# Performance work log

Hardware: AMD Instinct MI355X
Metric: run time of the kernel (lower is better)

## Reference

```python
import jax, jax.numpy as jnp
import numpy as np


def setup_inputs() -> dict:
    key = jax.random.key(0)
    k1, k2 = jax.random.split(key)
    b, feat = 8192, 256
    x = jax.random.normal(k1, (b, feat), dtype=jnp.float32)
    y = jax.random.randint(k2, (b,), 0, 100, dtype=jnp.int64)
    T = jnp.zeros((1,), dtype=jnp.float32)
    return {"x": x, "y": y, "T": T}


def reference(x, y, T):
    # SNNLoss.forward with inv=False, d=None, and no -1 labels in y
    b = x.shape[0]
    x = x / jnp.std(x, ddof=1)  # torch .std() is unbiased (ddof=1)

    # Pairwise Euclidean distance via Gram matrix (avoids [b,b,feat] blowup)
    sq = jnp.sum(x * x, axis=1)  # [b]
    d2 = jnp.maximum(sq[:, None] + sq[None, :] - 2.0 * (x @ x.T), 0.0)  # [b,b]
    eye = jnp.eye(b, dtype=bool)
    # diagonal is exactly 0 and masked out later; keep sqrt grad-safe there
    dist = jnp.where(eye, 0.0, jnp.sqrt(jnp.where(eye, 1.0, d2)))

    e_dist = -dist * jnp.power(jnp.float32(10.0), T[0])  # [b,b]
    neg_inf = jnp.float32(-jnp.inf)

    # denominator: all pairs except self
    den_dist = jnp.where(eye, neg_inf, e_dist)
    den = jax.scipy.special.logsumexp(den_dist, axis=1)  # [b]

    # numerator: same-label pairs except self
    m_num = (y[:, None] == y[None, :]) & ~eye  # [b,b]
    has = jnp.any(m_num, axis=1)  # rows with at least one positive
    num_dist = jnp.where(m_num, e_dist, neg_inf)
    # rows with no positives would give logsumexp = -inf; torch code zeroes
    # both num and den there. Substitute finite values, then zero the term.
    num = jax.scipy.special.logsumexp(jnp.where(has[:, None], num_dist, 0.0), axis=1)
    terms = jnp.where(has, num - den, 0.0)
    return -jnp.mean(terms)
```

## Files before the change

### kernel.cpp

```cpp
#include <hip/hip_runtime.h>

#define B_ROWS 8192
#define FEAT   256
#define NBLK   512
#define NJTILE 128

typedef float f32x4 __attribute__((ext_vector_type(4)));
typedef _Float16 f16x8 __attribute__((ext_vector_type(8)));

typedef const __attribute__((address_space(1))) unsigned int* gas_ptr;
typedef __attribute__((address_space(3))) unsigned int* las_ptr;

__device__ __forceinline__ void gload_lds16(const void* g, void* l) {
  __builtin_amdgcn_global_load_lds((gas_ptr)g, (las_ptr)l, 16, 0, 0);
}

__device__ __forceinline__ int Rc(int it) { return it * (129 - it); }

__global__ __launch_bounds__(256) void prep_kernel(
    const float* __restrict__ x, unsigned short* __restrict__ xh,
    float* __restrict__ sq, float* __restrict__ part_s,
    float* __restrict__ part_q, float* __restrict__ col_den,
    float* __restrict__ col_num, float* __restrict__ row_den,
    float* __restrict__ row_num)
{
  int tid = threadIdx.x;
  int l = tid & 63, wid = tid >> 6;
  int row = blockIdx.x * 4 + wid;
  const float4* xv = (const float4*)(x + (size_t)row * FEAT);
  float4 v = xv[l];
  ushort4 u;
  u.x = __builtin_bit_cast(unsigned short, (_Float16)v.x);
  u.y = __builtin_bit_cast(unsigned short, (_Float16)v.y);
  u.z = __builtin_bit_cast(unsigned short, (_Float16)v.z);
  u.w = __builtin_bit_cast(unsigned short, (_Float16)v.w);
  size_t off = ((size_t)(row >> 4) * 8 + (l >> 3)) * 1024
             + ((l >> 1) & 3) * 256 + (row & 15) * 16 + (l & 1) * 8;
  *(ushort4*)((char*)xh + off) = u;
  if (tid < 4) {
    int r4 = blockIdx.x * 4 + tid;
    col_den[r4] = 0.f; col_num[r4] = 0.f;
    row_den[r4] = 0.f; row_num[r4] = 0.f;
  }
  float ssq  = v.x*v.x + v.y*v.y + v.z*v.z + v.w*v.w;
  float ssum = v.x + v.y + v.z + v.w;
  #pragma unroll
  for (int m = 32; m; m >>= 1) {
    ssq  += __shfl_xor(ssq, m);
    ssum += __shfl_xor(ssum, m);
  }
  if (l == 0) sq[row] = ssq;
  __shared__ float red[8];
  if (l == 0) { red[wid*2] = ssum; red[wid*2+1] = ssq; }
  __syncthreads();
  if (tid == 0) {
    part_s[blockIdx.x] = red[0]+red[2]+red[4]+red[6];
    part_q[blockIdx.x] = red[1]+red[3]+red[5]+red[7];
  }
}

template<bool DIAG>
__device__ __forceinline__ void epilogue(
    const f32x4 (&acc)[2][4], const float* __restrict__ sq,
    const int* __restrict__ y, int j0, int l15, int l,
    int rbase, const float (&sqi)[8], const int (&yiv)[8],
    float (&sden)[8], float (&snum)[8], float nscale2,
    float* __restrict__ col_den, float* __restrict__ col_num)
{
  int jb = j0 + l15;
  float sqj[4]; int yj[4];
  #pragma unroll
  for (int cb = 0; cb < 4; ++cb) {
    int j = jb + cb*16;
    sqj[cb] = sq[j];
    yj[cb]  = y[j];
  }
  float cd[4], cn[4];
  if (!DIAG) {
    #pragma unroll
    for (int cb = 0; cb < 4; ++cb) { cd[cb] = 0.f; cn[cb] = 0.f; }
  }
  #pragma unroll
  for (int rb = 0; rb < 2; ++rb) {
    #pragma unroll
    for (int r = 0; r < 4; ++r) {
      float si = sqi[rb*4+r];
      int   ig = rbase + rb*16 + r;
      int   yi = yiv[rb*4+r];
      float dacc = 0.f, nacc = 0.f;
      #pragma unroll
      for (int cb = 0; cb < 4; ++cb) {
        float S  = acc[rb][cb][r];
        float d2 = fmaf(S, -2.0f, si + sqj[cb]);
        d2 = fmaxf(d2, 0.0f);
        float e  = __builtin_amdgcn_exp2f(__builtin_amdgcn_sqrtf(d2) * nscale2);
        bool same = (yi == yj[cb]);
        bool offd = !DIAG || (ig != jb + cb*16);
        dacc += offd ? e : 0.0f;
        nacc += (same && offd) ? e : 0.0f;
        if (!DIAG) {
          cd[cb] += e;
          cn[cb] += same ? e : 0.0f;
        }
      }
      sden[rb*4+r] += dacc;
      snum[rb*4+r] += nacc;
    }
  }
  if (!DIAG) {
    #pragma unroll
    for (int cb = 0; cb < 4; ++cb) {
      cd[cb] += __shfl_xor(cd[cb], 16);
      cd[cb] += __shfl_xor(cd[cb], 32);
      cn[cb] += __shfl_xor(cn[cb], 16);
      cn[cb] += __shfl_xor(cn[cb], 32);
    }
    if (l < 16) {
      #pragma unroll
      for (int cb = 0; cb < 4; ++cb) {
        atomicAdd(&col_den[j0 + cb*16 + l], cd[cb]);
        atomicAdd(&col_num[j0 + cb*16 + l], cn[cb]);
      }
    }
  }
}

__device__ __forceinline__ void process_run(
    int it, int jt0, int nt, const char* __restrict__ xb,
    const float* __restrict__ sq, const int* __restrict__ y,
    float nscale2, int l, int wid, int quad, int l15,
    float* __restrict__ row_den, float* __restrict__ row_num,
    float* __restrict__ col_den, float* __restrict__ col_num,
    char* lB)
{
  f16x8 areg[2][8];
  #pragma unroll
  for (int rb = 0; rb < 2; ++rb)
    #pragma unroll
    for (int kk = 0; kk < 8; ++kk)
      areg[rb][kk] = *(const f16x8*)(xb +
          ((size_t)(it*8 + wid*2 + rb) * 8 + kk) * 1024 + l*16);

  float sqi[8]; int yiv[8];
  int rbase = it*128 + wid*32 + quad*4;
  #pragma unroll
  for (int rb = 0; rb < 2; ++rb)
    #pragma unroll
    for (int r = 0; r < 4; ++r) {
      int idx = rbase + rb*16 + r;
      sqi[rb*4+r] = sq[idx];
      yiv[rb*4+r] = y[idx];
    }

  float sden[8], snum[8];
  #pragma unroll
  for (int v = 0; v < 8; ++v) { sden[v] = 0.f; snum[v] = 0.f; }
  f32x4 acc[2][4];
  const f32x4 zero4 = {0.f, 0.f, 0.f, 0.f};

  for (int n = 0; n < nt; ++n) {
    int jt = jt0 + n;

    __syncthreads();
    {
      const char* gB = xb + (size_t)jt * 32768;
      #pragma unroll
      for (int s = 0; s < 8; ++s) {
        int cc = wid*8 + s;
        gload_lds16(gB + cc*1024 + l*16, lB + cc*1024);
      }
    }

    if (n > 0) {
      int pjt = jt - 1;
      if ((pjt >> 1) == it)
        epilogue<true >(acc, sq, y, pjt*64, l15, l, rbase, sqi, yiv,
                        sden, snum, nscale2, col_den, col_num);
      else
        epilogue<false>(acc, sq, y, pjt*64, l15, l, rbase, sqi, yiv,
                        sden, snum, nscale2, col_den, col_num);
    }
    #pragma unroll
    for (int rb = 0; rb < 2; ++rb)
      #pragma unroll
      for (int cb = 0; cb < 4; ++cb)
        acc[rb][cb] = zero4;

    __syncthreads();

    #pragma unroll
    for (int kk = 0; kk < 8; ++kk) {
      f16x8 bv[4];
      #pragma unroll
      for (int cb = 0; cb < 4; ++cb)
        bv[cb] = *(const f16x8*)(lB + (cb*8 + kk)*1024 + l*16);
      #pragma unroll
      for (int rb = 0; rb < 2; ++rb)
        #pragma unroll
        for (int cb = 0; cb < 4; ++cb)
          acc[rb][cb] = __builtin_amdgcn_mfma_f32_16x16x32_f16(areg[rb][kk], bv[cb], acc[rb][cb], 0, 0, 0);
    }
  }
  {
    int pjt = jt0 + nt - 1;
    if ((pjt >> 1) == it)
      epilogue<true >(acc, sq, y, pjt*64, l15, l, rbase, sqi, yiv,
                      sden, snum, nscale2, col_den, col_num);
    else
      epilogue<false>(acc, sq, y, pjt*64, l15, l, rbase, sqi, yiv,
                      sden, snum, nscale2, col_den, col_num);
  }

  #pragma unroll
  for (int v = 0; v < 8; ++v) {
    #pragma unroll
    for (int m = 1; m <= 8; m <<= 1) {
      sden[v] += __shfl_xor(sden[v], m);
      snum[v] += __shfl_xor(snum[v], m);
    }
  }
  if (l15 == 0) {
    #pragma unroll
    for (int rb = 0; rb < 2; ++rb)
      #pragma unroll
      for (int r = 0; r < 4; ++r) {
        int ig = rbase + rb*16 + r;
        atomicAdd(&row_den[ig], sden[rb*4+r]);
        atomicAdd(&row_num[ig], snum[rb*4+r]);
      }
  }
}

__global__ __launch_bounds__(256, 2) void snn_main(
    const unsigned short* __restrict__ xh, const float* __restrict__ sq,
    const int* __restrict__ y, const float* __restrict__ T,
    const float* __restrict__ part_s, const float* __restrict__ part_q,
    float* __restrict__ row_den, float* __restrict__ row_num,
    float* __restrict__ col_den, float* __restrict__ col_num)
{
  __shared__ __align__(16) char lB[32768];
  int tid = threadIdx.x;
  int l = tid & 63, wid = tid >> 6;
  int quad = l >> 4, l15 = l & 15;
  int b = blockIdx.x;
  const char* xb = (const char*)xh;

  float s_acc = 0.f, q_acc = 0.f;
  #pragma unroll
  for (int t = 0; t < 32; ++t) {
    s_acc += part_s[l + 64*t];
    q_acc += part_q[l + 64*t];
  }
  #pragma unroll
  for (int m = 1; m <= 32; m <<= 1) {
    s_acc += __shfl_xor(s_acc, m);
    q_acc += __shfl_xor(q_acc, m);
  }
  const double n = (double)B_ROWS * FEAT;
  double var = ((double)q_acc - (double)s_acc*(double)s_acc/n) / (n - 1.0);
  float stdv = (float)sqrt(var);
  float p10  = __builtin_amdgcn_exp2f(T[0] * 3.3219280948873623f);
  float nscale2 = -(p10 * 1.4426950408889634f / stdv);

  int k    = (b * 65) >> 3;
  int kend = ((b + 1) * 65) >> 3;
  int it = (int)((129.0f - __builtin_amdgcn_sqrtf(16641.0f - 4.0f*(float)k)) * 0.5f);
  if (it < 0) it = 0;
  if (it > 63) it = 63;
  while (it < 63 && Rc(it + 1) <= k) ++it;
  while (it > 0 && Rc(it) > k) --it;

  while (k < kend) {
    int jt0  = 2*it + (k - Rc(it));
    int rowe = Rc(it + 1);
    int stop = (kend < rowe) ? kend : rowe;
    int nt   = stop - k;
    process_run(it, jt0, nt, xb, sq, y, nscale2, l, wid, quad, l15,
                row_den, row_num, col_den, col_num, lB);
    k = stop;
    ++it;
  }
}

__global__ __launch_bounds__(1024) void final_kernel(
    const float* __restrict__ row_den, const float* __restrict__ row_num,
    const float* __restrict__ col_den, const float* __restrict__ col_num,
    float* __restrict__ out)
{
  int tid = threadIdx.x;
  float tot = 0.f;
  #pragma unroll
  for (int rr = 0; rr < 8; ++rr) {
    int row = tid + 1024*rr;
    float den = row_den[row] + col_den[row];
    float num = row_num[row] + col_num[row];
    if (num > 0.f)
      tot += 0.6931471805599453f *
             (__builtin_amdgcn_logf(num) - __builtin_amdgcn_logf(den));
  }
  #pragma unroll
  for (int m = 32; m; m >>= 1) tot += __shfl_xor(tot, m);
  __shared__ float red[16];
  if ((tid & 63) == 0) red[tid >> 6] = tot;
  __syncthreads();
  if (tid == 0) {
    float s = 0.f;
    #pragma unroll
    for (int w = 0; w < 16; ++w) s += red[w];
    out[0] = -s / 8192.0f;
  }
}

extern "C" void kernel_launch(void* const* d_in, const int* in_sizes, int n_in,
                              void* d_out, int out_size, void* d_ws, size_t ws_size,
                              hipStream_t stream)
{
  (void)in_sizes; (void)n_in; (void)out_size; (void)ws_size;
  const float* x  = (const float*)d_in[0];
  const int* y    = (const int*)d_in[1];
  const float* T  = (const float*)d_in[2];
  char* ws = (char*)d_ws;
  float* part_s = (float*)(ws + 1024);
  float* part_q = (float*)(ws + 1024 + 8192);
  float* sq     = (float*)(ws + 32768);
  unsigned short* xh = (unsigned short*)(ws + 65536);
  float* col_den = (float*)(ws + 65536 + 4194304);
  float* col_num = col_den + B_ROWS;
  float* row_den = col_num + B_ROWS;
  float* row_num = row_den + B_ROWS;

  hipLaunchKernelGGL(prep_kernel, dim3(B_ROWS/4), dim3(256), 0, stream,
                     x, xh, sq, part_s, part_q, col_den, col_num,
                     row_den, row_num);
  hipLaunchKernelGGL(snn_main, dim3(NBLK), dim3(256), 0, stream,
                     xh, sq, y, T, part_s, part_q, row_den, row_num,
                     col_den, col_num);
  hipLaunchKernelGGL(final_kernel, dim3(1), dim3(1024), 0, stream,
                     row_den, row_num, col_den, col_num, (float*)d_out);
}
```

Before: 106.3 us.

## Fuse prep, main and final kernels into one persistent kernel with grid barriers

```diff
diff --git a/kernel.cpp b/kernel.cpp
--- a/kernel.cpp
+++ b/kernel.cpp
@@ -16,48 +16,6 @@
 }
 
 __device__ __forceinline__ int Rc(int it) { return it * (129 - it); }
-
-__global__ __launch_bounds__(256) void prep_kernel(
-    const float* __restrict__ x, unsigned short* __restrict__ xh,
-    float* __restrict__ sq, float* __restrict__ part_s,
-    float* __restrict__ part_q, float* __restrict__ col_den,
-    float* __restrict__ col_num, float* __restrict__ row_den,
-    float* __restrict__ row_num)
-{
-  int tid = threadIdx.x;
-  int l = tid & 63, wid = tid >> 6;
-  int row = blockIdx.x * 4 + wid;
-  const float4* xv = (const float4*)(x + (size_t)row * FEAT);
-  float4 v = xv[l];
-  ushort4 u;
-  u.x = __builtin_bit_cast(unsigned short, (_Float16)v.x);
-  u.y = __builtin_bit_cast(unsigned short, (_Float16)v.y);
-  u.z = __builtin_bit_cast(unsigned short, (_Float16)v.z);
-  u.w = __builtin_bit_cast(unsigned short, (_Float16)v.w);
-  size_t off = ((size_t)(row >> 4) * 8 + (l >> 3)) * 1024
-             + ((l >> 1) & 3) * 256 + (row & 15) * 16 + (l & 1) * 8;
-  *(ushort4*)((char*)xh + off) = u;
-  if (tid < 4) {
-    int r4 = blockIdx.x * 4 + tid;
-    col_den[r4] = 0.f; col_num[r4] = 0.f;
-    row_den[r4] = 0.f; row_num[r4] = 0.f;
-  }
-  float ssq  = v.x*v.x + v.y*v.y + v.z*v.z + v.w*v.w;
-  float ssum = v.x + v.y + v.z + v.w;
-  #pragma unroll
-  for (int m = 32; m; m >>= 1) {
-    ssq  += __shfl_xor(ssq, m);
-    ssum += __shfl_xor(ssum, m);
-  }
-  if (l == 0) sq[row] = ssq;
-  __shared__ float red[8];
-  if (l == 0) { red[wid*2] = ssum; red[wid*2+1] = ssq; }
-  __syncthreads();
-  if (tid == 0) {
-    part_s[blockIdx.x] = red[0]+red[2]+red[4]+red[6];
-    part_q[blockIdx.x] = red[1]+red[3]+red[5]+red[7];
-  }
-}
 
 template<bool DIAG>
 __device__ __forceinline__ void epilogue(
@@ -231,23 +189,71 @@
   }
 }
 
-__global__ __launch_bounds__(256, 2) void snn_main(
-    const unsigned short* __restrict__ xh, const float* __restrict__ sq,
-    const int* __restrict__ y, const float* __restrict__ T,
-    const float* __restrict__ part_s, const float* __restrict__ part_q,
+__global__ __launch_bounds__(256, 2) void snn_fused(
+    const float* __restrict__ x, unsigned short* __restrict__ xh,
+    float* __restrict__ sq, const int* __restrict__ y,
+    const float* __restrict__ T,
+    float* __restrict__ part_s, float* __restrict__ part_q,
     float* __restrict__ row_den, float* __restrict__ row_num,
-    float* __restrict__ col_den, float* __restrict__ col_num)
+    float* __restrict__ col_den, float* __restrict__ col_num,
+    unsigned* __restrict__ bar, float* __restrict__ out)
 {
   __shared__ __align__(16) char lB[32768];
+  __shared__ float red[8];
   int tid = threadIdx.x;
   int l = tid & 63, wid = tid >> 6;
   int quad = l >> 4, l15 = l & 15;
   int b = blockIdx.x;
   const char* xb = (const char*)xh;
 
+  float wsum = 0.f, wssq = 0.f;
+  #pragma unroll
+  for (int iter = 0; iter < 4; ++iter) {
+    int row = b*16 + iter*4 + wid;
+    float4 v = ((const float4*)(x + (size_t)row * FEAT))[l];
+    ushort4 u;
+    u.x = __builtin_bit_cast(unsigned short, (_Float16)v.x);
+    u.y = __builtin_bit_cast(unsigned short, (_Float16)v.y);
+    u.z = __builtin_bit_cast(unsigned short, (_Float16)v.z);
+    u.w = __builtin_bit_cast(unsigned short, (_Float16)v.w);
+    size_t off = ((size_t)(row >> 4) * 8 + (l >> 3)) * 1024
+               + ((l >> 1) & 3) * 256 + (row & 15) * 16 + (l & 1) * 8;
+    *(ushort4*)((char*)xh + off) = u;
+    float ssq  = v.x*v.x + v.y*v.y + v.z*v.z + v.w*v.w;
+    float ssum = v.x + v.y + v.z + v.w;
+    #pragma unroll
+    for (int m = 32; m; m >>= 1) {
+      ssq  += __shfl_xor(ssq, m);
+      ssum += __shfl_xor(ssum, m);
+    }
+    if (l == 0) sq[row] = ssq;
+    wsum += ssum; wssq += ssq;
+  }
+  if (tid < 16) {
+    int r = b*16 + tid;
+    row_den[r] = 0.f; row_num[r] = 0.f;
+    col_den[r] = 0.f; col_num[r] = 0.f;
+  }
+  if (l == 0) { red[wid*2] = wsum; red[wid*2+1] = wssq; }
+  __syncthreads();
+  if (tid == 0) {
+    part_s[b] = red[0]+red[2]+red[4]+red[6];
+    part_q[b] = red[1]+red[3]+red[5]+red[7];
+  }
+
+  __syncthreads();
+  if (tid == 0) {
+    __threadfence();
+    atomicAdd(&bar[0], 1u);
+    while (*(volatile unsigned*)&bar[0] < NBLK)
+      __builtin_amdgcn_s_sleep(2);
+    __threadfence();
+  }
+  __syncthreads();
+
   float s_acc = 0.f, q_acc = 0.f;
   #pragma unroll
-  for (int t = 0; t < 32; ++t) {
+  for (int t = 0; t < 8; ++t) {
     s_acc += part_s[l + 64*t];
     q_acc += part_q[l + 64*t];
   }
@@ -280,34 +286,36 @@
     k = stop;
     ++it;
   }
-}
-
-__global__ __launch_bounds__(1024) void final_kernel(
-    const float* __restrict__ row_den, const float* __restrict__ row_num,
-    const float* __restrict__ col_den, const float* __restrict__ col_num,
-    float* __restrict__ out)
-{
-  int tid = threadIdx.x;
-  float tot = 0.f;
-  #pragma unroll
-  for (int rr = 0; rr < 8; ++rr) {
-    int row = tid + 1024*rr;
-    float den = row_den[row] + col_den[row];
-    float num = row_num[row] + col_num[row];
-    if (num > 0.f)
-      tot += 0.6931471805599453f *
-             (__builtin_amdgcn_logf(num) - __builtin_amdgcn_logf(den));
-  }
-  #pragma unroll
-  for (int m = 32; m; m >>= 1) tot += __shfl_xor(tot, m);
-  __shared__ float red[16];
-  if ((tid & 63) == 0) red[tid >> 6] = tot;
+
   __syncthreads();
   if (tid == 0) {
-    float s = 0.f;
-    #pragma unroll
-    for (int w = 0; w < 16; ++w) s += red[w];
-    out[0] = -s / 8192.0f;
+    __threadfence();
+    atomicAdd(&bar[1], 1u);
+  }
+  if (b == 0) {
+    if (tid == 0) {
+      while (*(volatile unsigned*)&bar[1] < NBLK)
+        __builtin_amdgcn_s_sleep(2);
+      __threadfence();
+    }
+    __syncthreads();
+
+    float tot = 0.f;
+    #pragma unroll
+    for (int rr = 0; rr < 32; ++rr) {
+      int row = tid + 256*rr;
+      float den = row_den[row] + col_den[row];
+      float num = row_num[row] + col_num[row];
+      if (num > 0.f)
+        tot += 0.6931471805599453f *
+               (__builtin_amdgcn_logf(num) - __builtin_amdgcn_logf(den));
+    }
+    #pragma unroll
+    for (int m = 32; m; m >>= 1) tot += __shfl_xor(tot, m);
+    if (l == 0) red[wid] = tot;
+    __syncthreads();
+    if (tid == 0)
+      out[0] = -(red[0]+red[1]+red[2]+red[3]) / 8192.0f;
   }
 }
 
@@ -320,6 +328,7 @@
   const int* y    = (const int*)d_in[1];
   const float* T  = (const float*)d_in[2];
   char* ws = (char*)d_ws;
+  unsigned* bar  = (unsigned*)ws;
   float* part_s = (float*)(ws + 1024);
   float* part_q = (float*)(ws + 1024 + 8192);
   float* sq     = (float*)(ws + 32768);
@@ -329,12 +338,8 @@
   float* row_den = col_num + B_ROWS;
   float* row_num = row_den + B_ROWS;
 
-  hipLaunchKernelGGL(prep_kernel, dim3(B_ROWS/4), dim3(256), 0, stream,
-                     x, xh, sq, part_s, part_q, col_den, col_num,
-                     row_den, row_num);
-  hipLaunchKernelGGL(snn_main, dim3(NBLK), dim3(256), 0, stream,
-                     xh, sq, y, T, part_s, part_q, row_den, row_num,
-                     col_den, col_num);
-  hipLaunchKernelGGL(final_kernel, dim3(1), dim3(1024), 0, stream,
-                     row_den, row_num, col_den, col_num, (float*)d_out);
-}
+  hipMemsetAsync(ws, 0, 16, stream);
+  hipLaunchKernelGGL(snn_fused, dim3(NBLK), dim3(256), 0, stream,
+                     x, xh, sq, y, T, part_s, part_q,
+                     row_den, row_num, col_den, col_num, bar, (float*)d_out);
+}
```

Measured after the change: 167.2 us. +57.2%, slower.

## Double-buffer LDS B tiles to prefetch the next tile during compute

Applied to the files above, without the earlier changes.

```diff
diff --git a/kernel.cpp b/kernel.cpp
--- a/kernel.cpp
+++ b/kernel.cpp
@@ -125,13 +125,63 @@
   }
 }
 
-__device__ __forceinline__ void process_run(
+template<bool FIRST>
+__device__ __forceinline__ void tile_step(
+    int n, int nt, int jt0, int it, const char* __restrict__ xb,
+    const f16x8 (&areg)[2][8], const float* __restrict__ sq,
+    const int* __restrict__ y, float nscale2,
+    int l, int wid, int quad, int l15, int rbase,
+    const float (&sqi)[8], const int (&yiv)[8],
+    float (&sden)[8], float (&snum)[8],
+    float* __restrict__ col_den, float* __restrict__ col_num,
+    f32x4 (&acc)[2][4], char* cur, char* nxt)
+{
+  __syncthreads();
+  if (n + 1 < nt) {
+    const char* gB = xb + (size_t)(jt0 + n + 1) * 32768;
+    #pragma unroll
+    for (int s = 0; s < 8; ++s) {
+      int cc = wid*8 + s;
+      gload_lds16(gB + cc*1024 + l*16, nxt + cc*1024);
+    }
+  }
+  if (!FIRST) {
+    int pjt = jt0 + n - 1;
+    if ((pjt >> 1) == it)
+      epilogue<true >(acc, sq, y, pjt*64, l15, l, rbase, sqi, yiv,
+                      sden, snum, nscale2, col_den, col_num);
+    else
+      epilogue<false>(acc, sq, y, pjt*64, l15, l, rbase, sqi, yiv,
+                      sden, snum, nscale2, col_den, col_num);
+  }
+  const f32x4 zero4 = {0.f, 0.f, 0.f, 0.f};
+  #pragma unroll
+  for (int rb = 0; rb < 2; ++rb)
+    #pragma unroll
+    for (int cb = 0; cb < 4; ++cb)
+      acc[rb][cb] = zero4;
+
+  #pragma unroll
+  for (int kk = 0; kk < 8; ++kk) {
+    f16x8 bv[4];
+    #pragma unroll
+    for (int cb = 0; cb < 4; ++cb)
+      bv[cb] = *(const f16x8*)(cur + (cb*8 + kk)*1024 + l*16);
+    #pragma unroll
+    for (int rb = 0; rb < 2; ++rb)
+      #pragma unroll
+      for (int cb = 0; cb < 4; ++cb)
+        acc[rb][cb] = __builtin_amdgcn_mfma_f32_16x16x32_f16(areg[rb][kk], bv[cb], acc[rb][cb], 0, 0, 0);
+  }
+}
+
+__device__ void process_run(
     int it, int jt0, int nt, const char* __restrict__ xb,
     const float* __restrict__ sq, const int* __restrict__ y,
     float nscale2, int l, int wid, int quad, int l15,
     float* __restrict__ row_den, float* __restrict__ row_num,
     float* __restrict__ col_den, float* __restrict__ col_num,
-    char* lB)
+    char* lB0, char* lB1)
 {
   f16x8 areg[2][8];
   #pragma unroll
@@ -156,51 +206,38 @@
   #pragma unroll
   for (int v = 0; v < 8; ++v) { sden[v] = 0.f; snum[v] = 0.f; }
   f32x4 acc[2][4];
-  const f32x4 zero4 = {0.f, 0.f, 0.f, 0.f};
-
-  for (int n = 0; n < nt; ++n) {
-    int jt = jt0 + n;
-
-    __syncthreads();
-    {
-      const char* gB = xb + (size_t)jt * 32768;
-      #pragma unroll
-      for (int s = 0; s < 8; ++s) {
-        int cc = wid*8 + s;
-        gload_lds16(gB + cc*1024 + l*16, lB + cc*1024);
-      }
-    }
-
-    if (n > 0) {
-      int pjt = jt - 1;
-      if ((pjt >> 1) == it)
-        epilogue<true >(acc, sq, y, pjt*64, l15, l, rbase, sqi, yiv,
-                        sden, snum, nscale2, col_den, col_num);
-      else
-        epilogue<false>(acc, sq, y, pjt*64, l15, l, rbase, sqi, yiv,
-                        sden, snum, nscale2, col_den, col_num);
-    }
-    #pragma unroll
-    for (int rb = 0; rb < 2; ++rb)
-      #pragma unroll
-      for (int cb = 0; cb < 4; ++cb)
-        acc[rb][cb] = zero4;
-
-    __syncthreads();
-
-    #pragma unroll
-    for (int kk = 0; kk < 8; ++kk) {
-      f16x8 bv[4];
-      #pragma unroll
-      for (int cb = 0; cb < 4; ++cb)
-        bv[cb] = *(const f16x8*)(lB + (cb*8 + kk)*1024 + l*16);
-      #pragma unroll
-      for (int rb = 0; rb < 2; ++rb)
-        #pragma unroll
-        for (int cb = 0; cb < 4; ++cb)
-          acc[rb][cb] = __builtin_amdgcn_mfma_f32_16x16x32_f16(areg[rb][kk], bv[cb], acc[rb][cb], 0, 0, 0);
-    }
-  }
+
+  __syncthreads();
+  {
+    const char* gB = xb + (size_t)jt0 * 32768;
+    #pragma unroll
+    for (int s = 0; s < 8; ++s) {
+      int cc = wid*8 + s;
+      gload_lds16(gB + cc*1024 + l*16, lB0 + cc*1024);
+    }
+  }
+
+  int n = 0;
+  if (nt >= 1)
+    tile_step<true >(0, nt, jt0, it, xb, areg, sq, y, nscale2,
+                     l, wid, quad, l15, rbase, sqi, yiv, sden, snum,
+                     col_den, col_num, acc, lB0, lB1);
+  if (nt >= 2)
+    tile_step<false>(1, nt, jt0, it, xb, areg, sq, y, nscale2,
+                     l, wid, quad, l15, rbase, sqi, yiv, sden, snum,
+                     col_den, col_num, acc, lB1, lB0);
+  for (n = 2; n + 2 <= nt; n += 2) {
+    tile_step<false>(n,     nt, jt0, it, xb, areg, sq, y, nscale2,
+                     l, wid, quad, l15, rbase, sqi, yiv, sden, snum,
+                     col_den, col_num, acc, lB0, lB1);
+    tile_step<false>(n + 1, nt, jt0, it, xb, areg, sq, y, nscale2,
+                     l, wid, quad, l15, rbase, sqi, yiv, sden, snum,
+                     col_den, col_num, acc, lB1, lB0);
+  }
+  if (n < nt)
+    tile_step<false>(n, nt, jt0, it, xb, areg, sq, y, nscale2,
+                     l, wid, quad, l15, rbase, sqi, yiv, sden, snum,
+                     col_den, col_num, acc, lB0, lB1);
   {
     int pjt = jt0 + nt - 1;
     if ((pjt >> 1) == it)
@@ -238,7 +275,8 @@
     float* __restrict__ row_den, float* __restrict__ row_num,
     float* __restrict__ col_den, float* __restrict__ col_num)
 {
-  __shared__ __align__(16) char lB[32768];
+  __shared__ __align__(16) char lB0[32768];
+  __shared__ __align__(16) char lB1[32768];
   int tid = threadIdx.x;
   int l = tid & 63, wid = tid >> 6;
   int quad = l >> 4, l15 = l & 15;
@@ -276,7 +314,7 @@
     int stop = (kend < rowe) ? kend : rowe;
     int nt   = stop - k;
     process_run(it, jt0, nt, xb, sq, y, nscale2, l, wid, quad, l15,
-                row_den, row_num, col_den, col_num, lB);
+                row_den, row_num, col_den, col_num, lB0, lB1);
     k = stop;
     ++it;
   }
```

Result: slower. 122.5 us (+15.2%).

## Process pairs of column tiles per iteration with doubled LDS and accumulators

Applied to the files above, without the earlier changes.

```diff
diff --git a/kernel.cpp b/kernel.cpp
--- a/kernel.cpp
+++ b/kernel.cpp
@@ -59,26 +59,26 @@
   }
 }
 
-template<bool DIAG>
+template<int NCB, bool DIAG, bool COL>
 __device__ __forceinline__ void epilogue(
-    const f32x4 (&acc)[2][4], const float* __restrict__ sq,
+    const f32x4 (&acc)[2][8], const float* __restrict__ sq,
     const int* __restrict__ y, int j0, int l15, int l,
     int rbase, const float (&sqi)[8], const int (&yiv)[8],
     float (&sden)[8], float (&snum)[8], float nscale2,
     float* __restrict__ col_den, float* __restrict__ col_num)
 {
   int jb = j0 + l15;
-  float sqj[4]; int yj[4];
-  #pragma unroll
-  for (int cb = 0; cb < 4; ++cb) {
+  float sqj[NCB]; int yj[NCB];
+  #pragma unroll
+  for (int cb = 0; cb < NCB; ++cb) {
     int j = jb + cb*16;
     sqj[cb] = sq[j];
     yj[cb]  = y[j];
   }
-  float cd[4], cn[4];
-  if (!DIAG) {
-    #pragma unroll
-    for (int cb = 0; cb < 4; ++cb) { cd[cb] = 0.f; cn[cb] = 0.f; }
+  float cd[NCB], cn[NCB];
+  if (COL) {
+    #pragma unroll
+    for (int cb = 0; cb < NCB; ++cb) { cd[cb] = 0.f; cn[cb] = 0.f; }
   }
   #pragma unroll
   for (int rb = 0; rb < 2; ++rb) {
@@ -89,7 +89,7 @@
       int   yi = yiv[rb*4+r];
       float dacc = 0.f, nacc = 0.f;
       #pragma unroll
-      for (int cb = 0; cb < 4; ++cb) {
+      for (int cb = 0; cb < NCB; ++cb) {
         float S  = acc[rb][cb][r];
         float d2 = fmaf(S, -2.0f, si + sqj[cb]);
         d2 = fmaxf(d2, 0.0f);
@@ -98,7 +98,7 @@
         bool offd = !DIAG || (ig != jb + cb*16);
         dacc += offd ? e : 0.0f;
         nacc += (same && offd) ? e : 0.0f;
-        if (!DIAG) {
+        if (COL) {
           cd[cb] += e;
           cn[cb] += same ? e : 0.0f;
         }
@@ -107,9 +107,9 @@
       snum[rb*4+r] += nacc;
     }
   }
-  if (!DIAG) {
-    #pragma unroll
-    for (int cb = 0; cb < 4; ++cb) {
+  if (COL) {
+    #pragma unroll
+    for (int cb = 0; cb < NCB; ++cb) {
       cd[cb] += __shfl_xor(cd[cb], 16);
       cd[cb] += __shfl_xor(cd[cb], 32);
       cn[cb] += __shfl_xor(cn[cb], 16);
@@ -117,7 +117,7 @@
     }
     if (l < 16) {
       #pragma unroll
-      for (int cb = 0; cb < 4; ++cb) {
+      for (int cb = 0; cb < NCB; ++cb) {
         atomicAdd(&col_den[j0 + cb*16 + l], cd[cb]);
         atomicAdd(&col_num[j0 + cb*16 + l], cn[cb]);
       }
@@ -125,7 +125,32 @@
   }
 }
 
-__device__ __forceinline__ void process_run(
+__device__ __forceinline__ void do_epilogue(
+    bool ppair, bool pdiag, const f32x4 (&acc)[2][8],
+    const float* __restrict__ sq, const int* __restrict__ y,
+    int j0, int l15, int l, int rbase,
+    const float (&sqi)[8], const int (&yiv)[8],
+    float (&sden)[8], float (&snum)[8], float nscale2,
+    float* __restrict__ col_den, float* __restrict__ col_num)
+{
+  if (ppair) {
+    if (pdiag)
+      epilogue<8, true , false>(acc, sq, y, j0, l15, l, rbase, sqi, yiv,
+                                sden, snum, nscale2, col_den, col_num);
+    else
+      epilogue<8, false, true >(acc, sq, y, j0, l15, l, rbase, sqi, yiv,
+                                sden, snum, nscale2, col_den, col_num);
+  } else {
+    if (pdiag)
+      epilogue<4, true , false>(acc, sq, y, j0, l15, l, rbase, sqi, yiv,
+                                sden, snum, nscale2, col_den, col_num);
+    else
+      epilogue<4, false, true >(acc, sq, y, j0, l15, l, rbase, sqi, yiv,
+                                sden, snum, nscale2, col_den, col_num);
+  }
+}
+
+__device__ void process_run(
     int it, int jt0, int nt, const char* __restrict__ xb,
     const float* __restrict__ sq, const int* __restrict__ y,
     float nscale2, int l, int wid, int quad, int l15,
@@ -155,68 +180,85 @@
   float sden[8], snum[8];
   #pragma unroll
   for (int v = 0; v < 8; ++v) { sden[v] = 0.f; snum[v] = 0.f; }
-  f32x4 acc[2][4];
+  f32x4 acc[2][8];
   const f32x4 zero4 = {0.f, 0.f, 0.f, 0.f};
 
-  for (int n = 0; n < nt; ++n) {
-    int jt = jt0 + n;
+  int pjt = -1; bool ppair = false, pdiag = false;
+  int m = 0;
+  while (m < nt) {
+    int jt = jt0 + m;
+    bool pair = ((((jt - 2*it) & 1) == 0) && (m + 1 < nt));
 
     __syncthreads();
     {
       const char* gB = xb + (size_t)jt * 32768;
-      #pragma unroll
-      for (int s = 0; s < 8; ++s) {
-        int cc = wid*8 + s;
-        gload_lds16(gB + cc*1024 + l*16, lB + cc*1024);
-      }
-    }
-
-    if (n > 0) {
-      int pjt = jt - 1;
-      if ((pjt >> 1) == it)
-        epilogue<true >(acc, sq, y, pjt*64, l15, l, rbase, sqi, yiv,
-                        sden, snum, nscale2, col_den, col_num);
-      else
-        epilogue<false>(acc, sq, y, pjt*64, l15, l, rbase, sqi, yiv,
-                        sden, snum, nscale2, col_den, col_num);
-    }
+      if (pair) {
+        #pragma unroll
+        for (int s = 0; s < 16; ++s) {
+          int cc = wid*16 + s;
+          gload_lds16(gB + cc*1024 + l*16, lB + cc*1024);
+        }
+      } else {
+        #pragma unroll
+        for (int s = 0; s < 8; ++s) {
+          int cc = wid*8 + s;
+          gload_lds16(gB + cc*1024 + l*16, lB + cc*1024);
+        }
+      }
+    }
+
+    if (pjt >= 0)
+      do_epilogue(ppair, pdiag, acc, sq, y, pjt*64, l15, l, rbase,
+                  sqi, yiv, sden, snum, nscale2, col_den, col_num);
     #pragma unroll
     for (int rb = 0; rb < 2; ++rb)
       #pragma unroll
-      for (int cb = 0; cb < 4; ++cb)
+      for (int cb = 0; cb < 8; ++cb)
         acc[rb][cb] = zero4;
 
     __syncthreads();
 
-    #pragma unroll
-    for (int kk = 0; kk < 8; ++kk) {
-      f16x8 bv[4];
-      #pragma unroll
-      for (int cb = 0; cb < 4; ++cb)
-        bv[cb] = *(const f16x8*)(lB + (cb*8 + kk)*1024 + l*16);
-      #pragma unroll
-      for (int rb = 0; rb < 2; ++rb)
+    if (pair) {
+      #pragma unroll
+      for (int kk = 0; kk < 8; ++kk) {
+        f16x8 bv[8];
+        #pragma unroll
+        for (int cb = 0; cb < 8; ++cb)
+          bv[cb] = *(const f16x8*)(lB + (cb*8 + kk)*1024 + l*16);
+        #pragma unroll
+        for (int rb = 0; rb < 2; ++rb)
+          #pragma unroll
+          for (int cb = 0; cb < 8; ++cb)
+            acc[rb][cb] = __builtin_amdgcn_mfma_f32_16x16x32_f16(areg[rb][kk], bv[cb], acc[rb][cb], 0, 0, 0);
+      }
+    } else {
+      #pragma unroll
+      for (int kk = 0; kk < 8; ++kk) {
+        f16x8 bv[4];
         #pragma unroll
         for (int cb = 0; cb < 4; ++cb)
-          acc[rb][cb] = __builtin_amdgcn_mfma_f32_16x16x32_f16(areg[rb][kk], bv[cb], acc[rb][cb], 0, 0, 0);
-    }
-  }
-  {
-    int pjt = jt0 + nt - 1;
-    if ((pjt >> 1) == it)
-      epilogue<true >(acc, sq, y, pjt*64, l15, l, rbase, sqi, yiv,
-                      sden, snum, nscale2, col_den, col_num);
-    else
-      epilogue<false>(acc, sq, y, pjt*64, l15, l, rbase, sqi, yiv,
-                      sden, snum, nscale2, col_den, col_num);
-  }
+          bv[cb] = *(const f16x8*)(lB + (cb*8 + kk)*1024 + l*16);
+        #pragma unroll
+        for (int rb = 0; rb < 2; ++rb)
+          #pragma unroll
+          for (int cb = 0; cb < 4; ++cb)
+            acc[rb][cb] = __builtin_amdgcn_mfma_f32_16x16x32_f16(areg[rb][kk], bv[cb], acc[rb][cb], 0, 0, 0);
+      }
+    }
+
+    pdiag = pair ? (jt == 2*it) : ((jt >> 1) == it);
+    pjt = jt; ppair = pair;
+    m += pair ? 2 : 1;
+  }
+  do_epilogue(ppair, pdiag, acc, sq, y, pjt*64, l15, l, rbase,
+              sqi, yiv, sden, snum, nscale2, col_den, col_num);
 
   #pragma unroll
   for (int v = 0; v < 8; ++v) {
     #pragma unroll
-    for (int m = 1; m <= 8; m <<= 1) {
-      sden[v] += __shfl_xor(sden[v], m);
-      snum[v] += __shfl_xor(snum[v], m);
+    for (int m2 = 1; m2 <= 8; m2 <<= 1) {
+      sden[v] += __shfl_xor(sden[v], m2);
+      snum[v] += __shfl_xor(snum[v], m2);
     }
   }
   if (l15 == 0) {
@@ -238,7 +280,7 @@
     float* __restrict__ row_den, float* __restrict__ row_num,
     float* __restrict__ col_den, float* __restrict__ col_num)
 {
-  __shared__ __align__(16) char lB[32768];
+  __shared__ __align__(16) char lB[65536];
   int tid = threadIdx.x;
   int l = tid & 63, wid = tid >> 6;
   int quad = l >> 4, l15 = l & 15;
```

New measurement: 165.4 us. 1.56x slower.
